# Kernel optimization log

Measured on AMD Instinct MI355X. Metric: run time of the kernel, lower is better.

Reference implementation:

```python
import jax, jax.numpy as jnp
import numpy as np

NUM_USERS = 200_000
NUM_ITEMS = 100_000
N = NUM_USERS + NUM_ITEMS
D = 32
E = 9_600_000
N_LAYERS = 3


def setup_inputs() -> dict:
    key = jax.random.key(0)
    k1, k2, k3, k4, k5 = jax.random.split(key, 5)
    rows = jax.random.randint(k1, (E,), 0, N, dtype=jnp.int32)
    cols = jax.random.randint(k2, (E,), 0, N, dtype=jnp.int32)
    # normalized-adjacency-like positive values
    vals = jax.random.uniform(k3, (E,), dtype=jnp.float32) * 0.05
    # xavier-uniform-ish embedding init
    bound = float(np.sqrt(6.0 / (NUM_USERS + D)))
    user_w = jax.random.uniform(k4, (NUM_USERS, D), dtype=jnp.float32,
                                minval=-bound, maxval=bound)
    bound_i = float(np.sqrt(6.0 / (NUM_ITEMS + D)))
    item_w = jax.random.uniform(k5, (NUM_ITEMS, D), dtype=jnp.float32,
                                minval=-bound_i, maxval=bound_i)
    return {"rows": rows, "cols": cols, "vals": vals,
            "user_w": user_w, "item_w": item_w}


def _spmm(rows, cols, vals, x):
    # A_hat @ x for COO A_hat: gather source features, scale, scatter-add to rows.
    msgs = vals[:, None] * x[cols]                 # [E, D]
    return jax.ops.segment_sum(msgs, rows, num_segments=N)  # [N, D]


def reference(rows, cols, vals, user_w, item_w):
    x0 = jnp.concatenate([user_w, item_w], axis=0)  # [N, D]
    x = x0
    acc = x0
    for _ in range(N_LAYERS):
        x = _spmm(rows, cols, vals, x)
        acc = acc + x
    x_mean = acc / (N_LAYERS + 1)                   # mean over layer stack
    users = x_mean[:NUM_USERS]
    items = x_mean[NUM_USERS:]
    return (users, items)
```

## Files before the change

### kernel.cpp

```cpp
#include <hip/hip_runtime.h>
#include <hip/hip_fp16.h>
#include <stdint.h>

#define NUM_USERS 200000
#define NUM_ITEMS 100000
#define NN (NUM_USERS + NUM_ITEMS)
#define D 32
#define NE 9600000
#define TOTAL (NN * D)

#define RPB2 128
#define B2 ((NN + RPB2 - 1) / RPB2)
#define CAP 5120

#define CSH 12
#define NC ((NN + (1 << CSH) - 1) >> CSH)
#define FPC 32
#define BPC 9

#define TPB_A 1024
#define EPT 16
#define EPB_A (TPB_A * EPT)

#define TPB_H 1024
#define EPT_H 32
#define EPB_H (TPB_H * EPT_H)
#define NB_H ((NE + EPB_H - 1) / EPB_H)

__global__ __launch_bounds__(256) void init_x0(
    const float4* __restrict__ user_w, const float4* __restrict__ item_w,
    ushort4* __restrict__ x0h) {
    int i = blockIdx.x * 256 + threadIdx.x;
    const int total4 = TOTAL / 4;
    const int ub4 = (NUM_USERS * D) / 4;
    if (i < total4) {
        float4 v = (i < ub4) ? user_w[i] : item_w[i - ub4];
        ushort4 h;
        h.x = __half_as_ushort(__float2half(v.x));
        h.y = __half_as_ushort(__float2half(v.y));
        h.z = __half_as_ushort(__float2half(v.z));
        h.w = __half_as_ushort(__float2half(v.w));
        x0h[i] = h;
    }
}

__global__ __launch_bounds__(TPB_H) void bucket_hist(
    const int4* __restrict__ rows4, int* __restrict__ bcounts) {
    __shared__ int hist[B2];
    int tid = threadIdx.x;
    for (int i = tid; i < B2; i += TPB_H) hist[i] = 0;
    __syncthreads();
    int base4 = blockIdx.x * (EPB_H / 4);
    #pragma unroll
    for (int k = 0; k < EPT_H / 4; ++k) {
        int i4 = base4 + k * TPB_H + tid;
        if (i4 < NE / 4) {
            int4 r = rows4[i4];
            atomicAdd(&hist[r.x >> 7], 1);
            atomicAdd(&hist[r.y >> 7], 1);
            atomicAdd(&hist[r.z >> 7], 1);
            atomicAdd(&hist[r.w >> 7], 1);
        }
    }
    __syncthreads();
    for (int b = tid; b < B2; b += TPB_H) {
        int c = hist[b];
        if (c) atomicAdd(&bcounts[b], c);
    }
}

__global__ __launch_bounds__(1024) void scan_buckets(
    const int* __restrict__ bcounts, int* __restrict__ bstart,
    int* __restrict__ bfill, int* __restrict__ cfill) {
    __shared__ int lds[1024];
    int t = threadIdx.x;
    int v[4];
    int s = 0;
    #pragma unroll
    for (int k = 0; k < 4; ++k) {
        int b = t * 4 + k;
        v[k] = (b < B2) ? bcounts[b] : 0;
        s += v[k];
    }
    lds[t] = s;
    __syncthreads();
    for (int off = 1; off < 1024; off <<= 1) {
        int u = (t >= off) ? lds[t - off] : 0;
        __syncthreads();
        lds[t] += u;
        __syncthreads();
    }
    int ex = lds[t] - s;
    #pragma unroll
    for (int k = 0; k < 4; ++k) {
        int b = t * 4 + k;
        if (b < B2) {
            bstart[b] = ex;
            bfill[b] = ex;
            if ((b & (FPC - 1)) == 0) cfill[b >> 5] = ex;
        }
        ex += v[k];
    }
    if (t == 1023) bstart[B2] = ex;
}

__global__ __launch_bounds__(TPB_A) void partition_coarse(
    const int4* __restrict__ rows4, const int4* __restrict__ cols4,
    const float4* __restrict__ vals4, int* __restrict__ cfill,
    int2* __restrict__ temp1) {
    __shared__ int2 stage[EPB_A];
    __shared__ int hist[NC];
    __shared__ int bnd[NC + 1];
    __shared__ int dlt[NC];
    __shared__ int sc[128];
    int tid = threadIdx.x;
    if (tid < NC) hist[tid] = 0;
    __syncthreads();

    int base4 = blockIdx.x * (EPB_A / 4);
    int keys[EPT]; int vls[EPT]; int crk[EPT];

    #pragma unroll
    for (int k = 0; k < EPT / 4; ++k) {
        int i4 = base4 + k * TPB_A + tid;
        if (i4 < NE / 4) {
            int4 r = rows4[i4];
            int4 c = cols4[i4];
            float4 v = vals4[i4];
            int c0 = r.x >> CSH, c1 = r.y >> CSH, c2 = r.z >> CSH, c3 = r.w >> CSH;
            keys[k*4+0] = ((r.x & 4095) << 19) | c.x; vls[k*4+0] = __float_as_int(v.x);
            crk[k*4+0] = (c0 << 13) | atomicAdd(&hist[c0], 1);
            keys[k*4+1] = ((r.y & 4095) << 19) | c.y; vls[k*4+1] = __float_as_int(v.y);
            crk[k*4+1] = (c1 << 13) | atomicAdd(&hist[c1], 1);
            keys[k*4+2] = ((r.z & 4095) << 19) | c.z; vls[k*4+2] = __float_as_int(v.z);
            crk[k*4+2] = (c2 << 13) | atomicAdd(&hist[c2], 1);
            keys[k*4+3] = ((r.w & 4095) << 19) | c.w; vls[k*4+3] = __float_as_int(v.w);
            crk[k*4+3] = (c3 << 13) | atomicAdd(&hist[c3], 1);
        }
    }
    __syncthreads();
    if (tid < 128) sc[tid] = (tid < NC) ? hist[tid] : 0;
    __syncthreads();
    #pragma unroll
    for (int off = 1; off < 128; off <<= 1) {
        int u = (tid >= off && tid < 128) ? sc[tid - off] : 0;
        __syncthreads();
        if (tid < 128) sc[tid] += u;
        __syncthreads();
    }
    if (tid < NC) {
        int cnt = hist[tid];
        int ex = sc[tid] - cnt;
        bnd[tid] = ex;
        dlt[tid] = (cnt ? atomicAdd(&cfill[tid], cnt) : 0) - ex;
    }
    if (tid == 0) bnd[NC] = sc[NC - 1];
    __syncthreads();
    #pragma unroll
    for (int k = 0; k < EPT / 4; ++k) {
        int i4 = base4 + k * TPB_A + tid;
        if (i4 < NE / 4) {
            #pragma unroll
            for (int j = 0; j < 4; ++j) {
                int e = k * 4 + j;
                int p = bnd[crk[e] >> 13] + (crk[e] & 0x1FFF);
                stage[p] = make_int2(keys[e], vls[e]);
            }
        }
    }
    __syncthreads();
    int ntot = bnd[NC];
    for (int j = tid; j < ntot; j += TPB_A) {
        int lo = 0, hi = NC;
        while (hi - lo > 1) { int mid = (lo + hi) >> 1; if (bnd[mid] <= j) lo = mid; else hi = mid; }
        temp1[j + dlt[lo]] = stage[j];
    }
}

__global__ __launch_bounds__(TPB_A) void partition_fine(
    const int2* __restrict__ temp1, const int* __restrict__ bstart,
    int* __restrict__ bfill, int2* __restrict__ colval) {
    __shared__ int2 stage[EPB_A];
    __shared__ int hist[FPC];
    __shared__ int bnd[FPC + 1];
    __shared__ int dlt[FPC];
    __shared__ int sc[FPC];
    int c = blockIdx.x / BPC;
    int seg = blockIdx.x % BPC;
    int cs = bstart[c * FPC];
    int ce = bstart[min((c + 1) * FPC, B2)];
    int base = cs + seg * EPB_A;
    int n = ce - base;
    if (n <= 0) return;
    if (n > EPB_A) n = EPB_A;
    int tid = threadIdx.x;
    if (tid < FPC) hist[tid] = 0;
    __syncthreads();
    int keys[EPT]; int vls[EPT]; int frk[EPT];
    #pragma unroll
    for (int k = 0; k < EPT; ++k) {
        int idx = k * TPB_A + tid;
        if (idx < n) {
            int2 e = temp1[base + idx];
            int f = (e.x >> 26) & 31;
            keys[k] = e.x; vls[k] = e.y;
            frk[k] = (f << 13) | atomicAdd(&hist[f], 1);
        }
    }
    __syncthreads();
    if (tid < FPC) sc[tid] = hist[tid];
    __syncthreads();
    #pragma unroll
    for (int off = 1; off < FPC; off <<= 1) {
        int u = (tid >= off && tid < FPC) ? sc[tid - off] : 0;
        __syncthreads();
        if (tid < FPC) sc[tid] += u;
        __syncthreads();
    }
    if (tid < FPC) {
        int cnt = hist[tid];
        int ex = sc[tid] - cnt;
        bnd[tid] = ex;
        dlt[tid] = (cnt ? atomicAdd(&bfill[c * FPC + tid], cnt) : 0) - ex;
    }
    if (tid == 0) bnd[FPC] = sc[FPC - 1];
    __syncthreads();
    #pragma unroll
    for (int k = 0; k < EPT; ++k) {
        int idx = k * TPB_A + tid;
        if (idx < n) {
            int p = bnd[frk[k] >> 13] + (frk[k] & 0x1FFF);
            int rl = (keys[k] >> 19) & 127;
            stage[p] = make_int2((rl << 19) | (keys[k] & 0x7FFFF), vls[k]);
        }
    }
    __syncthreads();
    for (int j = tid; j < n; j += TPB_A) {
        int lo = 0, hi = FPC;
        while (hi - lo > 1) { int mid = (lo + hi) >> 1; if (bnd[mid] <= j) lo = mid; else hi = mid; }
        colval[j + dlt[lo]] = stage[j];
    }
}

__global__ __launch_bounds__(256) void sort_bucket2(
    const int* __restrict__ bstart, int* __restrict__ row_start,
    int2* __restrict__ colval, int2* __restrict__ scratch) {
    __shared__ int2 stage[CAP];
    __shared__ int lstart[RPB2];
    __shared__ int lfill[RPB2];
    int b = blockIdx.x;
    int row0 = b * RPB2;
    int rcount = NN - row0; if (rcount > RPB2) rcount = RPB2;
    int tid = threadIdx.x;
    int s = bstart[b];
    int count = bstart[b + 1] - s;

    if (tid < RPB2) lfill[tid] = 0;
    __syncthreads();

    for (int i = tid; i < count; i += 256) {
        int rl = colval[s + i].x >> 19;
        atomicAdd(&lfill[rl], 1);
    }
    __syncthreads();

    int val = (tid < RPB2) ? lfill[tid] : 0;
    if (tid < RPB2) lstart[tid] = val;
    __syncthreads();
    for (int off = 1; off < RPB2; off <<= 1) {
        int u = (tid >= off && tid < RPB2) ? lstart[tid - off] : 0;
        __syncthreads();
        if (tid < RPB2) lstart[tid] += u;
        __syncthreads();
    }
    int ex = (tid < RPB2) ? lstart[tid] - val : 0;
    if (tid < RPB2) {
        lstart[tid] = ex;
        lfill[tid] = 0;
        if (tid < rcount) row_start[row0 + tid] = s + ex;
    }
    if (b == 0 && tid == 0) row_start[NN] = NE;
    __syncthreads();

    if (count <= CAP) {
        for (int i = tid; i < count; i += 256) {
            int2 e = colval[s + i];
            int rl = e.x >> 19;
            int pos = lstart[rl] + atomicAdd(&lfill[rl], 1);
            stage[pos] = make_int2(e.x & 0x7FFFF, e.y);
        }
        __syncthreads();
        for (int i = tid; i < count; i += 256) colval[s + i] = stage[i];
    } else {
        for (int i = tid; i < count; i += 256) scratch[s + i] = colval[s + i];
        __syncthreads();
        for (int i = tid; i < count; i += 256) {
            int2 e = scratch[s + i];
            int rl = e.x >> 19;
            int pos = lstart[rl] + atomicAdd(&lfill[rl], 1);
            colval[s + pos] = make_int2(e.x & 0x7FFFF, e.y);
        }
    }
}

__device__ __forceinline__ float2 h2f(uint32_t u) {
    return __half22float2(*(__half2*)&u);
}

template <bool LAST>
__global__ __launch_bounds__(256) void spmm_csr(
    const int* __restrict__ row_start, const int2* __restrict__ colval,
    const __half* __restrict__ xh, __half* __restrict__ yh,
    const uint2* __restrict__ x0u, const uint2* __restrict__ x1u,
    const uint2* __restrict__ x2u, float4* __restrict__ out) {
    int lane = threadIdx.x & 63;
    int grp = lane >> 3;
    int fq = lane & 7;
    int row = (blockIdx.x * 256 + threadIdx.x) >> 6;
    if (row >= NN) return;
    int s = row_start[row];
    int e = row_start[row + 1];
    const int64_t* cv8 = (const int64_t*)colval;
    float a0 = 0.f, a1 = 0.f, a2 = 0.f, a3 = 0.f;
    int i = s;
    for (; i + 32 <= e; i += 32) {
        int64_t p0 = __builtin_nontemporal_load(&cv8[i + grp]);
        int64_t p1 = __builtin_nontemporal_load(&cv8[i + 8 + grp]);
        int64_t p2 = __builtin_nontemporal_load(&cv8[i + 16 + grp]);
        int64_t p3 = __builtin_nontemporal_load(&cv8[i + 24 + grp]);
        uint2 h0 = *(const uint2*)(xh + (size_t)(uint32_t)p0 * D + fq * 4);
        uint2 h1 = *(const uint2*)(xh + (size_t)(uint32_t)p1 * D + fq * 4);
        uint2 h2 = *(const uint2*)(xh + (size_t)(uint32_t)p2 * D + fq * 4);
        uint2 h3 = *(const uint2*)(xh + (size_t)(uint32_t)p3 * D + fq * 4);
        float v0 = __int_as_float((int)(p0 >> 32));
        float v1 = __int_as_float((int)(p1 >> 32));
        float v2 = __int_as_float((int)(p2 >> 32));
        float v3 = __int_as_float((int)(p3 >> 32));
        float2 f;
        f = h2f(h0.x); a0 += v0 * f.x; a1 += v0 * f.y;
        f = h2f(h0.y); a2 += v0 * f.x; a3 += v0 * f.y;
        f = h2f(h1.x); a0 += v1 * f.x; a1 += v1 * f.y;
        f = h2f(h1.y); a2 += v1 * f.x; a3 += v1 * f.y;
        f = h2f(h2.x); a0 += v2 * f.x; a1 += v2 * f.y;
        f = h2f(h2.y); a2 += v2 * f.x; a3 += v2 * f.y;
        f = h2f(h3.x); a0 += v3 * f.x; a1 += v3 * f.y;
        f = h2f(h3.y); a2 += v3 * f.x; a3 += v3 * f.y;
    }
    if (i < e) {
        int last = e - 1;
        int i0 = i + grp,      c0 = (i0 < e) ? i0 : last;
        int i1 = i + 8 + grp,  c1 = (i1 < e) ? i1 : last;
        int i2 = i + 16 + grp, c2 = (i2 < e) ? i2 : last;
        int i3 = i + 24 + grp, c3 = (i3 < e) ? i3 : last;
        int64_t p0 = __builtin_nontemporal_load(&cv8[c0]);
        int64_t p1 = __builtin_nontemporal_load(&cv8[c1]);
        int64_t p2 = __builtin_nontemporal_load(&cv8[c2]);
        int64_t p3 = __builtin_nontemporal_load(&cv8[c3]);
        uint2 h0 = *(const uint2*)(xh + (size_t)(uint32_t)p0 * D + fq * 4);
        uint2 h1 = *(const uint2*)(xh + (size_t)(uint32_t)p1 * D + fq * 4);
        uint2 h2 = *(const uint2*)(xh + (size_t)(uint32_t)p2 * D + fq * 4);
        uint2 h3 = *(const uint2*)(xh + (size_t)(uint32_t)p3 * D + fq * 4);
        float v0 = (i0 < e) ? __int_as_float((int)(p0 >> 32)) : 0.f;
        float v1 = (i1 < e) ? __int_as_float((int)(p1 >> 32)) : 0.f;
        float v2 = (i2 < e) ? __int_as_float((int)(p2 >> 32)) : 0.f;
        float v3 = (i3 < e) ? __int_as_float((int)(p3 >> 32)) : 0.f;
        float2 f;
        f = h2f(h0.x); a0 += v0 * f.x; a1 += v0 * f.y;
        f = h2f(h0.y); a2 += v0 * f.x; a3 += v0 * f.y;
        f = h2f(h1.x); a0 += v1 * f.x; a1 += v1 * f.y;
        f = h2f(h1.y); a2 += v1 * f.x; a3 += v1 * f.y;
        f = h2f(h2.x); a0 += v2 * f.x; a1 += v2 * f.y;
        f = h2f(h2.y); a2 += v2 * f.x; a3 += v2 * f.y;
        f = h2f(h3.x); a0 += v3 * f.x; a1 += v3 * f.y;
        f = h2f(h3.y); a2 += v3 * f.x; a3 += v3 * f.y;
    }
    #pragma unroll
    for (int m = 8; m <= 32; m <<= 1) {
        a0 += __shfl_xor(a0, m, 64);
        a1 += __shfl_xor(a1, m, 64);
        a2 += __shfl_xor(a2, m, 64);
        a3 += __shfl_xor(a3, m, 64);
    }
    if (lane < 8) {
        if (!LAST) {
            size_t idx = (size_t)row * D + lane * 4;
            __half2 h01 = __float22half2_rn(make_float2(a0, a1));
            __half2 h23 = __float22half2_rn(make_float2(a2, a3));
            *(uint2*)(yh + idx) = make_uint2(*(uint32_t*)&h01, *(uint32_t*)&h23);
        } else {
            int gi = row * 8 + lane;
            uint2 u0 = x0u[gi], u1 = x1u[gi], u2 = x2u[gi];
            float2 f0a = h2f(u0.x), f0b = h2f(u0.y);
            float2 f1a = h2f(u1.x), f1b = h2f(u1.y);
            float2 f2a = h2f(u2.x), f2b = h2f(u2.y);
            out[gi] = make_float4(
                (f0a.x + f1a.x + f2a.x + a0) * 0.25f,
                (f0a.y + f1a.y + f2a.y + a1) * 0.25f,
                (f0b.x + f1b.x + f2b.x + a2) * 0.25f,
                (f0b.y + f1b.y + f2b.y + a3) * 0.25f);
        }
    }
}

extern "C" void kernel_launch(void* const* d_in, const int* in_sizes, int n_in,
                              void* d_out, int out_size, void* d_ws, size_t ws_size,
                              hipStream_t stream) {
    const int*   rows   = (const int*)d_in[0];
    const int*   cols   = (const int*)d_in[1];
    const float* vals   = (const float*)d_in[2];
    const float* user_w = (const float*)d_in[3];
    const float* item_w = (const float*)d_in[4];

    float* acc = (float*)d_out;

    __half* x0h = (__half*)d_ws;
    __half* x1h = x0h + (size_t)TOTAL;
    __half* x2h = x1h + (size_t)TOTAL;
    int2*  temp1 = (int2*)d_ws;
    int2*  colval = (int2*)((char*)d_ws + 2ull * (size_t)TOTAL * sizeof(float));
    int*   bcounts = (int*)(colval + (size_t)NE);
    int*   bstart = bcounts + B2;
    int*   bfill = bstart + (B2 + 1);
    int*   cfill = bfill + B2;
    int*   row_start = cfill + NC;

    const int vec_blocks   = (TOTAL / 4 + 255) / 256;
    const int partA_blocks = (NE + EPB_A - 1) / EPB_A;
    const int partF_blocks = NC * BPC;
    const int row_blocks   = (NN + 3) / 4;

    hipMemsetAsync(bcounts, 0, (size_t)B2 * sizeof(int), stream);
    bucket_hist<<<NB_H, TPB_H, 0, stream>>>((const int4*)rows, bcounts);
    scan_buckets<<<1, 1024, 0, stream>>>(bcounts, bstart, bfill, cfill);
    partition_coarse<<<partA_blocks, TPB_A, 0, stream>>>(
        (const int4*)rows, (const int4*)cols, (const float4*)vals, cfill, temp1);
    partition_fine<<<partF_blocks, TPB_A, 0, stream>>>(
        (const int2*)temp1, bstart, bfill, colval);
    sort_bucket2<<<B2, 256, 0, stream>>>(bstart, row_start, colval, temp1);

    init_x0<<<vec_blocks, 256, 0, stream>>>(
        (const float4*)user_w, (const float4*)item_w, (ushort4*)x0h);

    spmm_csr<false><<<row_blocks, 256, 0, stream>>>(
        row_start, colval, x0h, x1h, nullptr, nullptr, nullptr, nullptr);
    spmm_csr<false><<<row_blocks, 256, 0, stream>>>(
        row_start, colval, x1h, x2h, nullptr, nullptr, nullptr, nullptr);
    spmm_csr<true ><<<row_blocks, 256, 0, stream>>>(
        row_start, colval, x2h, nullptr, (const uint2*)x0h, (const uint2*)x1h,
        (const uint2*)x2h, (float4*)acc);
}
```

Baseline: 809.9 us.

## Replace two-pass coarse/fine partition with single direct bucket partition

Merges the coarse (4096-row) and fine (128-row) partition kernels into one kernel that scatters edges straight into their 2344 final 128-row buckets. Each block keeps a full per-bucket histogram in shared memory and runs a 1024-thread scan over three buckets per thread. This removes a full read/write pass over the 9.6M edges and one launch. sort_bucket2 now caches the bucket in shared memory during counting, so it reads global memory once. In exchange, the global atomics on bfill per block rise sharply, the final scatter writes are less coalesced (about 7 edges per bucket per block), and the binary search is deeper.

```diff
diff --git a/kernel.cpp b/kernel.cpp
--- a/kernel.cpp
+++ b/kernel.cpp
@@ -12,11 +12,6 @@
 #define RPB2 128
 #define B2 ((NN + RPB2 - 1) / RPB2)
 #define CAP 5120
-
-#define CSH 12
-#define NC ((NN + (1 << CSH) - 1) >> CSH)
-#define FPC 32
-#define BPC 9
 
 #define TPB_A 1024
 #define EPT 16
@@ -71,7 +66,7 @@
 
 __global__ __launch_bounds__(1024) void scan_buckets(
     const int* __restrict__ bcounts, int* __restrict__ bstart,
-    int* __restrict__ bfill, int* __restrict__ cfill) {
+    int* __restrict__ bfill) {
     __shared__ int lds[1024];
     int t = threadIdx.x;
     int v[4];
@@ -94,27 +89,22 @@
     #pragma unroll
     for (int k = 0; k < 4; ++k) {
         int b = t * 4 + k;
-        if (b < B2) {
-            bstart[b] = ex;
-            bfill[b] = ex;
-            if ((b & (FPC - 1)) == 0) cfill[b >> 5] = ex;
-        }
+        if (b < B2) { bstart[b] = ex; bfill[b] = ex; }
         ex += v[k];
     }
     if (t == 1023) bstart[B2] = ex;
 }
 
-__global__ __launch_bounds__(TPB_A) void partition_coarse(
+__global__ __launch_bounds__(TPB_A) void partition_direct(
     const int4* __restrict__ rows4, const int4* __restrict__ cols4,
-    const float4* __restrict__ vals4, int* __restrict__ cfill,
-    int2* __restrict__ temp1) {
+    const float4* __restrict__ vals4, int* __restrict__ bfill,
+    int2* __restrict__ colval) {
     __shared__ int2 stage[EPB_A];
-    __shared__ int hist[NC];
-    __shared__ int bnd[NC + 1];
-    __shared__ int dlt[NC];
-    __shared__ int sc[128];
+    __shared__ int bnd[B2 + 1];
+    __shared__ int dlt[B2];
+    __shared__ int sc[1024];
     int tid = threadIdx.x;
-    if (tid < NC) hist[tid] = 0;
+    for (int i = tid; i < B2 + 1; i += TPB_A) bnd[i] = 0;
     __syncthreads();
 
     int base4 = blockIdx.x * (EPB_A / 4);
@@ -127,34 +117,48 @@
             int4 r = rows4[i4];
             int4 c = cols4[i4];
             float4 v = vals4[i4];
-            int c0 = r.x >> CSH, c1 = r.y >> CSH, c2 = r.z >> CSH, c3 = r.w >> CSH;
-            keys[k*4+0] = ((r.x & 4095) << 19) | c.x; vls[k*4+0] = __float_as_int(v.x);
-            crk[k*4+0] = (c0 << 13) | atomicAdd(&hist[c0], 1);
-            keys[k*4+1] = ((r.y & 4095) << 19) | c.y; vls[k*4+1] = __float_as_int(v.y);
-            crk[k*4+1] = (c1 << 13) | atomicAdd(&hist[c1], 1);
-            keys[k*4+2] = ((r.z & 4095) << 19) | c.z; vls[k*4+2] = __float_as_int(v.z);
-            crk[k*4+2] = (c2 << 13) | atomicAdd(&hist[c2], 1);
-            keys[k*4+3] = ((r.w & 4095) << 19) | c.w; vls[k*4+3] = __float_as_int(v.w);
-            crk[k*4+3] = (c3 << 13) | atomicAdd(&hist[c3], 1);
-        }
-    }
-    __syncthreads();
-    if (tid < 128) sc[tid] = (tid < NC) ? hist[tid] : 0;
-    __syncthreads();
-    #pragma unroll
-    for (int off = 1; off < 128; off <<= 1) {
-        int u = (tid >= off && tid < 128) ? sc[tid - off] : 0;
-        __syncthreads();
-        if (tid < 128) sc[tid] += u;
-        __syncthreads();
-    }
-    if (tid < NC) {
-        int cnt = hist[tid];
-        int ex = sc[tid] - cnt;
-        bnd[tid] = ex;
-        dlt[tid] = (cnt ? atomicAdd(&cfill[tid], cnt) : 0) - ex;
-    }
-    if (tid == 0) bnd[NC] = sc[NC - 1];
+            int b0 = r.x >> 7, b1 = r.y >> 7, b2 = r.z >> 7, b3 = r.w >> 7;
+            keys[k*4+0] = ((r.x & 127) << 19) | c.x; vls[k*4+0] = __float_as_int(v.x);
+            crk[k*4+0] = (b0 << 13) | atomicAdd(&bnd[b0], 1);
+            keys[k*4+1] = ((r.y & 127) << 19) | c.y; vls[k*4+1] = __float_as_int(v.y);
+            crk[k*4+1] = (b1 << 13) | atomicAdd(&bnd[b1], 1);
+            keys[k*4+2] = ((r.z & 127) << 19) | c.z; vls[k*4+2] = __float_as_int(v.z);
+            crk[k*4+2] = (b2 << 13) | atomicAdd(&bnd[b2], 1);
+            keys[k*4+3] = ((r.w & 127) << 19) | c.w; vls[k*4+3] = __float_as_int(v.w);
+            crk[k*4+3] = (b3 << 13) | atomicAdd(&bnd[b3], 1);
+        }
+    }
+    __syncthreads();
+    int c0 = 0, c1 = 0, c2 = 0;
+    {
+        int b = tid * 3;
+        if (b     < B2) c0 = bnd[b];
+        if (b + 1 < B2) c1 = bnd[b + 1];
+        if (b + 2 < B2) c2 = bnd[b + 2];
+    }
+    int psum = c0 + c1 + c2;
+    sc[tid] = psum;
+    __syncthreads();
+    for (int off = 1; off < 1024; off <<= 1) {
+        int u = (tid >= off) ? sc[tid - off] : 0;
+        __syncthreads();
+        sc[tid] += u;
+        __syncthreads();
+    }
+    {
+        int ex = sc[tid] - psum;
+        int b = tid * 3;
+        #pragma unroll
+        for (int j = 0; j < 3; ++j) {
+            int cnt = (j == 0) ? c0 : (j == 1) ? c1 : c2;
+            if (b + j < B2) {
+                bnd[b + j] = ex;
+                dlt[b + j] = (cnt ? atomicAdd(&bfill[b + j], cnt) : 0) - ex;
+            }
+            ex += cnt;
+        }
+    }
+    if (tid == 1023) bnd[B2] = sc[1023];
     __syncthreads();
     #pragma unroll
     for (int k = 0; k < EPT / 4; ++k) {
@@ -169,74 +173,9 @@
         }
     }
     __syncthreads();
-    int ntot = bnd[NC];
+    int ntot = bnd[B2];
     for (int j = tid; j < ntot; j += TPB_A) {
-        int lo = 0, hi = NC;
-        while (hi - lo > 1) { int mid = (lo + hi) >> 1; if (bnd[mid] <= j) lo = mid; else hi = mid; }
-        temp1[j + dlt[lo]] = stage[j];
-    }
-}
-
-__global__ __launch_bounds__(TPB_A) void partition_fine(
-    const int2* __restrict__ temp1, const int* __restrict__ bstart,
-    int* __restrict__ bfill, int2* __restrict__ colval) {
-    __shared__ int2 stage[EPB_A];
-    __shared__ int hist[FPC];
-    __shared__ int bnd[FPC + 1];
-    __shared__ int dlt[FPC];
-    __shared__ int sc[FPC];
-    int c = blockIdx.x / BPC;
-    int seg = blockIdx.x % BPC;
-    int cs = bstart[c * FPC];
-    int ce = bstart[min((c + 1) * FPC, B2)];
-    int base = cs + seg * EPB_A;
-    int n = ce - base;
-    if (n <= 0) return;
-    if (n > EPB_A) n = EPB_A;
-    int tid = threadIdx.x;
-    if (tid < FPC) hist[tid] = 0;
-    __syncthreads();
-    int keys[EPT]; int vls[EPT]; int frk[EPT];
-    #pragma unroll
-    for (int k = 0; k < EPT; ++k) {
-        int idx = k * TPB_A + tid;
-        if (idx < n) {
-            int2 e = temp1[base + idx];
-            int f = (e.x >> 26) & 31;
-            keys[k] = e.x; vls[k] = e.y;
-            frk[k] = (f << 13) | atomicAdd(&hist[f], 1);
-        }
-    }
-    __syncthreads();
-    if (tid < FPC) sc[tid] = hist[tid];
-    __syncthreads();
-    #pragma unroll
-    for (int off = 1; off < FPC; off <<= 1) {
-        int u = (tid >= off && tid < FPC) ? sc[tid - off] : 0;
-        __syncthreads();
-        if (tid < FPC) sc[tid] += u;
-        __syncthreads();
-    }
-    if (tid < FPC) {
-        int cnt = hist[tid];
-        int ex = sc[tid] - cnt;
-        bnd[tid] = ex;
-        dlt[tid] = (cnt ? atomicAdd(&bfill[c * FPC + tid], cnt) : 0) - ex;
-    }
-    if (tid == 0) bnd[FPC] = sc[FPC - 1];
-    __syncthreads();
-    #pragma unroll
-    for (int k = 0; k < EPT; ++k) {
-        int idx = k * TPB_A + tid;
-        if (idx < n) {
-            int p = bnd[frk[k] >> 13] + (frk[k] & 0x1FFF);
-            int rl = (keys[k] >> 19) & 127;
-            stage[p] = make_int2((rl << 19) | (keys[k] & 0x7FFFF), vls[k]);
-        }
-    }
-    __syncthreads();
-    for (int j = tid; j < n; j += TPB_A) {
-        int lo = 0, hi = FPC;
+        int lo = 0, hi = B2;
         while (hi - lo > 1) { int mid = (lo + hi) >> 1; if (bnd[mid] <= j) lo = mid; else hi = mid; }
         colval[j + dlt[lo]] = stage[j];
     }
@@ -245,7 +184,8 @@
 __global__ __launch_bounds__(256) void sort_bucket2(
     const int* __restrict__ bstart, int* __restrict__ row_start,
     int2* __restrict__ colval, int2* __restrict__ scratch) {
-    __shared__ int2 stage[CAP];
+    __shared__ int2 sin[CAP];
+    __shared__ int2 sout[CAP];
     __shared__ int lstart[RPB2];
     __shared__ int lfill[RPB2];
     int b = blockIdx.x;
@@ -258,41 +198,61 @@
     if (tid < RPB2) lfill[tid] = 0;
     __syncthreads();
 
-    for (int i = tid; i < count; i += 256) {
-        int rl = colval[s + i].x >> 19;
-        atomicAdd(&lfill[rl], 1);
-    }
-    __syncthreads();
-
-    int val = (tid < RPB2) ? lfill[tid] : 0;
-    if (tid < RPB2) lstart[tid] = val;
-    __syncthreads();
-    for (int off = 1; off < RPB2; off <<= 1) {
-        int u = (tid >= off && tid < RPB2) ? lstart[tid - off] : 0;
-        __syncthreads();
-        if (tid < RPB2) lstart[tid] += u;
-        __syncthreads();
-    }
-    int ex = (tid < RPB2) ? lstart[tid] - val : 0;
-    if (tid < RPB2) {
-        lstart[tid] = ex;
-        lfill[tid] = 0;
-        if (tid < rcount) row_start[row0 + tid] = s + ex;
-    }
-    if (b == 0 && tid == 0) row_start[NN] = NE;
-    __syncthreads();
-
     if (count <= CAP) {
         for (int i = tid; i < count; i += 256) {
             int2 e = colval[s + i];
+            sin[i] = e;
+            atomicAdd(&lfill[e.x >> 19], 1);
+        }
+        __syncthreads();
+        int val = (tid < RPB2) ? lfill[tid] : 0;
+        if (tid < RPB2) lstart[tid] = val;
+        __syncthreads();
+        for (int off = 1; off < RPB2; off <<= 1) {
+            int u = (tid >= off && tid < RPB2) ? lstart[tid - off] : 0;
+            __syncthreads();
+            if (tid < RPB2) lstart[tid] += u;
+            __syncthreads();
+        }
+        int ex = (tid < RPB2) ? lstart[tid] - val : 0;
+        if (tid < RPB2) {
+            lstart[tid] = ex;
+            lfill[tid] = 0;
+            if (tid < rcount) row_start[row0 + tid] = s + ex;
+        }
+        if (b == 0 && tid == 0) row_start[NN] = NE;
+        __syncthreads();
+        for (int i = tid; i < count; i += 256) {
+            int2 e = sin[i];
             int rl = e.x >> 19;
             int pos = lstart[rl] + atomicAdd(&lfill[rl], 1);
-            stage[pos] = make_int2(e.x & 0x7FFFF, e.y);
-        }
-        __syncthreads();
-        for (int i = tid; i < count; i += 256) colval[s + i] = stage[i];
+            sout[pos] = make_int2(e.x & 0x7FFFF, e.y);
+        }
+        __syncthreads();
+        for (int i = tid; i < count; i += 256) colval[s + i] = sout[i];
     } else {
-        for (int i = tid; i < count; i += 256) scratch[s + i] = colval[s + i];
+        for (int i = tid; i < count; i += 256) {
+            int2 e = colval[s + i];
+            scratch[s + i] = e;
+            atomicAdd(&lfill[e.x >> 19], 1);
+        }
+        __syncthreads();
+        int val = (tid < RPB2) ? lfill[tid] : 0;
+        if (tid < RPB2) lstart[tid] = val;
+        __syncthreads();
+        for (int off = 1; off < RPB2; off <<= 1) {
+            int u = (tid >= off && tid < RPB2) ? lstart[tid - off] : 0;
+            __syncthreads();
+            if (tid < RPB2) lstart[tid] += u;
+            __syncthreads();
+        }
+        int ex = (tid < RPB2) ? lstart[tid] - val : 0;
+        if (tid < RPB2) {
+            lstart[tid] = ex;
+            lfill[tid] = 0;
+            if (tid < rcount) row_start[row0 + tid] = s + ex;
+        }
+        if (b == 0 && tid == 0) row_start[NN] = NE;
         __syncthreads();
         for (int i = tid; i < count; i += 256) {
             int2 e = scratch[s + i];
@@ -416,27 +376,23 @@
     __half* x0h = (__half*)d_ws;
     __half* x1h = x0h + (size_t)TOTAL;
     __half* x2h = x1h + (size_t)TOTAL;
-    int2*  temp1 = (int2*)d_ws;
+    int2*  scratch = (int2*)d_ws;
     int2*  colval = (int2*)((char*)d_ws + 2ull * (size_t)TOTAL * sizeof(float));
     int*   bcounts = (int*)(colval + (size_t)NE);
     int*   bstart = bcounts + B2;
     int*   bfill = bstart + (B2 + 1);
-    int*   cfill = bfill + B2;
-    int*   row_start = cfill + NC;
+    int*   row_start = bfill + B2;
 
     const int vec_blocks   = (TOTAL / 4 + 255) / 256;
     const int partA_blocks = (NE + EPB_A - 1) / EPB_A;
-    const int partF_blocks = NC * BPC;
     const int row_blocks   = (NN + 3) / 4;
 
     hipMemsetAsync(bcounts, 0, (size_t)B2 * sizeof(int), stream);
     bucket_hist<<<NB_H, TPB_H, 0, stream>>>((const int4*)rows, bcounts);
-    scan_buckets<<<1, 1024, 0, stream>>>(bcounts, bstart, bfill, cfill);
-    partition_coarse<<<partA_blocks, TPB_A, 0, stream>>>(
-        (const int4*)rows, (const int4*)cols, (const float4*)vals, cfill, temp1);
-    partition_fine<<<partF_blocks, TPB_A, 0, stream>>>(
-        (const int2*)temp1, bstart, bfill, colval);
-    sort_bucket2<<<B2, 256, 0, stream>>>(bstart, row_start, colval, temp1);
+    scan_buckets<<<1, 1024, 0, stream>>>(bcounts, bstart, bfill);
+    partition_direct<<<partA_blocks, TPB_A, 0, stream>>>(
+        (const int4*)rows, (const int4*)cols, (const float4*)vals, bfill, colval);
+    sort_bucket2<<<B2, 256, 0, stream>>>(bstart, row_start, colval, scratch);
 
     init_x0<<<vec_blocks, 256, 0, stream>>>(
         (const float4*)user_w, (const float4*)item_w, (ushort4*)x0h);
```

Result: slower. 843.1 us (+4.1%).
